# Performance work log

Hardware: AMD Instinct MI355X
Metric: run time of the kernel (lower is better)

## Reference

```python
import math
import jax, jax.numpy as jnp
import numpy as np

VOCAB = 50257
HIDDEN = 768
TYPE_VOCAB = 2
MAX_POS = 5000
EPS = 1e-12


def sinusoidal_pe(max_len, dim):
    # matches SinPositionalEncoding: pe[:,0::2]=sin(pos*div), pe[:,1::2]=cos(pos*div)
    position = np.arange(max_len, dtype=np.float32)[:, None]
    div_term = np.exp(np.arange(0, dim, 2, dtype=np.float32) * -(math.log(10000.0) / dim))
    pe = np.zeros((max_len, dim), dtype=np.float32)
    pe[:, 0::2] = np.sin(position * div_term)
    pe[:, 1::2] = np.cos(position * div_term)
    return jnp.asarray(pe)  # [max_len, dim]


def setup_inputs() -> dict:
    key = jax.random.key(0)
    k1, k2, k3, k4, k5 = jax.random.split(key, 5)
    B, N = 8, 4096
    return {
        "input_ids": jax.random.randint(k1, (B, N), 0, VOCAB, dtype=jnp.int64 if jax.config.jax_enable_x64 else jnp.int32),
        "tok_struct_vec": jax.random.randint(k2, (B, N, 3), 0, MAX_POS, dtype=jnp.int32),
        "token_type_ids": jax.random.randint(k3, (B, N), 0, TYPE_VOCAB, dtype=jnp.int32),
        "word_emb": jax.random.normal(k4, (VOCAB, HIDDEN), dtype=jnp.float32) * 0.02,
        "type_emb": jax.random.normal(k5, (TYPE_VOCAB, HIDDEN), dtype=jnp.float32) * 0.02,
        "gamma": jnp.ones((HIDDEN,), dtype=jnp.float32),
        "beta": jnp.zeros((HIDDEN,), dtype=jnp.float32),
    }


def reference(input_ids, tok_struct_vec, token_type_ids, word_emb, type_emb, gamma, beta):
    B, N = input_ids.shape
    pe = sinusoidal_pe(MAX_POS, HIDDEN)  # [max_pos, H]

    words = word_emb[input_ids]                      # [B,N,H] gather
    types = type_emb[token_type_ids]                 # [B,N,H] gather
    pos = jnp.broadcast_to(pe[:N][None], (B, N, HIDDEN))  # pe[:, :n].expand

    # compute_se: vectorized gather of pe rows by structure positions
    para = pe[tok_struct_vec[:, :, 0]]               # [B,N,H]
    sent = pe[tok_struct_vec[:, :, 1]]
    tok = pe[tok_struct_vec[:, :, 2]]
    struct = para + sent + tok                       # tok_se_comb_mode == 'sum'

    emb = words + pos + types + struct
    # BertLayerNorm (eps=1e-12); dropout is identity in eval
    mean = jnp.mean(emb, axis=-1, keepdims=True)
    var = jnp.mean(jnp.square(emb - mean), axis=-1, keepdims=True)
    out = (emb - mean) / jnp.sqrt(var + EPS) * gamma + beta
    return out
```

## Files before the change

### kernel.cpp

```cpp
#include <hip/hip_runtime.h>
#include <hip/hip_fp16.h>
#include <cstdint>
#include <cmath>

#define HIDDEN   768
#define NPAIR    (HIDDEN / 2)
#define SEQ_N    4096
#define LN_EPS   1e-12f
#define N_HI     80
#define N_LO     64

typedef float    f4v __attribute__((ext_vector_type(4)));
typedef _Float16 h4v __attribute__((ext_vector_type(4)));

__global__ __launch_bounds__(256) void pe_tables_kernel(__half2* __restrict__ T) {
    const int total = (N_HI + N_LO) * NPAIR;
    int idx = blockIdx.x * 256 + threadIdx.x;
    if (idx >= total) return;
    int r = idx / NPAIR;
    int i = idx % NPAIR;
    const float L = logf(10000.0f) / (float)HIDDEN;
    float div = expf(-2.0f * (float)i * L);
    int p = (r < N_HI) ? (r << 6) : (r - N_HI);
    float s, c;
    sincosf((float)p * div, &s, &c);
    T[idx] = __floats2half2_rn(s, c);
}

__device__ __forceinline__ void pe_acc(float4& x, const h4v a, const h4v b) {
    const float sA0 = (float)a.x, cA0 = (float)a.y, sA1 = (float)a.z, cA1 = (float)a.w;
    const float sB0 = (float)b.x, cB0 = (float)b.y, sB1 = (float)b.z, cB1 = (float)b.w;
    x.x = fmaf(sA0, cB0, fmaf(cA0, sB0, x.x));
    x.y = fmaf(cA0, cB0, fmaf(-sA0, sB0, x.y));
    x.z = fmaf(sA1, cB1, fmaf(cA1, sB1, x.z));
    x.w = fmaf(cA1, cB1, fmaf(-sA1, sB1, x.w));
}

__global__ __launch_bounds__(256) void emb_ln_kernel(
    const int*     __restrict__ ids,
    const int*     __restrict__ svec,
    const int*     __restrict__ tt,
    const float*   __restrict__ word_emb,
    const float*   __restrict__ type_emb,
    const float*   __restrict__ gamma,
    const float*   __restrict__ beta,
    const __half2* __restrict__ T,
    float*         __restrict__ out,
    int n_tokens)
{
    const int wave = threadIdx.x >> 6;
    const int lane = threadIdx.x & 63;
    const int tok  = blockIdx.x * 4 + wave;
    if (tok >= n_tokens) return;

    const int n  = tok & (SEQ_N - 1);
    const int id = ids[tok];
    const int ty = tt[tok];
    const int p0 = svec[tok * 3 + 0];
    const int p1 = svec[tok * 3 + 1];
    const int p2 = svec[tok * 3 + 2];

    const float4* wrow = reinterpret_cast<const float4*>(word_emb + (size_t)id * HIDDEN);
    const float4* trow = reinterpret_cast<const float4*>(type_emb + (size_t)ty * HIDDEN);

    #define T1ROW(p) reinterpret_cast<const h4v*>(T + (size_t)((p) >> 6) * NPAIR)
    #define T2ROW(p) reinterpret_cast<const h4v*>(T + (size_t)(N_HI + ((p) & 63)) * NPAIR)
    const h4v* A0 = T1ROW(n),  *B0 = T2ROW(n);
    const h4v* A1 = T1ROW(p0), *B1 = T2ROW(p0);
    const h4v* A2 = T1ROW(p1), *B2 = T2ROW(p1);
    const h4v* A3 = T1ROW(p2), *B3 = T2ROW(p2);
    #undef T1ROW
    #undef T2ROW

    float4 acc[3];
    float s = 0.0f, ss = 0.0f;

    #pragma unroll
    for (int k = 0; k < 3; ++k) {
        const int d4 = lane + 64 * k;

        float4 w = wrow[d4];
        float4 t = trow[d4];
        h4v a0 = A0[d4], b0 = B0[d4];
        h4v a1 = A1[d4], b1 = B1[d4];
        h4v a2 = A2[d4], b2 = B2[d4];
        h4v a3 = A3[d4], b3 = B3[d4];

        float4 x;
        x.x = w.x + t.x; x.y = w.y + t.y; x.z = w.z + t.z; x.w = w.w + t.w;
        pe_acc(x, a0, b0);
        pe_acc(x, a1, b1);
        pe_acc(x, a2, b2);
        pe_acc(x, a3, b3);

        acc[k] = x;
        s  += x.x + x.y + x.z + x.w;
        ss += x.x * x.x + x.y * x.y + x.z * x.z + x.w * x.w;
    }

    #pragma unroll
    for (int off = 1; off < 64; off <<= 1) {
        s  += __shfl_xor(s,  off);
        ss += __shfl_xor(ss, off);
    }

    const float mean = s * (1.0f / (float)HIDDEN);
    const float var  = ss * (1.0f / (float)HIDDEN) - mean * mean;
    const float inv  = rsqrtf(var + LN_EPS);

    const float4* g4 = reinterpret_cast<const float4*>(gamma);
    const float4* b4 = reinterpret_cast<const float4*>(beta);
    float4* orow = reinterpret_cast<float4*>(out + (size_t)tok * HIDDEN);

    #pragma unroll
    for (int k = 0; k < 3; ++k) {
        const int d4 = lane + 64 * k;
        const float4 g = g4[d4];
        const float4 b = b4[d4];
        const float4 x = acc[k];
        float4 r;
        r.x = (x.x - mean) * inv * g.x + b.x;
        r.y = (x.y - mean) * inv * g.y + b.y;
        r.z = (x.z - mean) * inv * g.z + b.z;
        r.w = (x.w - mean) * inv * g.w + b.w;
        orow[d4] = r;
    }
}

extern "C" void kernel_launch(void* const* d_in, const int* in_sizes, int n_in,
                              void* d_out, int out_size, void* d_ws, size_t ws_size,
                              hipStream_t stream) {
    const int*   ids      = (const int*)d_in[0];
    const int*   svec     = (const int*)d_in[1];
    const int*   tt       = (const int*)d_in[2];
    const float* word_emb = (const float*)d_in[3];
    const float* type_emb = (const float*)d_in[4];
    const float* gamma    = (const float*)d_in[5];
    const float* beta     = (const float*)d_in[6];
    float*       out      = (float*)d_out;

    const int n_tokens = in_sizes[0];
    const int grid_main = (n_tokens + 3) / 4;

    __half2* T = (__half2*)d_ws;
    const int total_tab = (N_HI + N_LO) * NPAIR;
    pe_tables_kernel<<<(total_tab + 255) / 256, 256, 0, stream>>>(T);
    emb_ln_kernel<<<grid_main, 256, 0, stream>>>(
        ids, svec, tt, word_emb, type_emb, gamma, beta, T, out, n_tokens);
}
```

Before: 53.25 us.

## Use persistent grid-stride waves with prefetch of next token's indices

```diff
diff --git a/kernel.cpp b/kernel.cpp
--- a/kernel.cpp
+++ b/kernel.cpp
@@ -9,6 +9,7 @@
 #define LN_EPS   1e-12f
 #define N_HI     80
 #define N_LO     64
+#define NBLK     2048
 
 typedef float    f4v __attribute__((ext_vector_type(4)));
 typedef _Float16 h4v __attribute__((ext_vector_type(4)));
@@ -36,7 +37,7 @@
     x.w = fmaf(cA1, cB1, fmaf(-sA1, sB1, x.w));
 }
 
-__global__ __launch_bounds__(256) void emb_ln_kernel(
+__global__ __launch_bounds__(256, 8) void emb_ln_kernel(
     const int*     __restrict__ ids,
     const int*     __restrict__ svec,
     const int*     __restrict__ tt,
@@ -50,80 +51,93 @@
 {
     const int wave = threadIdx.x >> 6;
     const int lane = threadIdx.x & 63;
-    const int tok  = blockIdx.x * 4 + wave;
+    const int nw   = NBLK * 4;
+    int tok = blockIdx.x * 4 + wave;
     if (tok >= n_tokens) return;
 
-    const int n  = tok & (SEQ_N - 1);
-    const int id = ids[tok];
-    const int ty = tt[tok];
-    const int p0 = svec[tok * 3 + 0];
-    const int p1 = svec[tok * 3 + 1];
-    const int p2 = svec[tok * 3 + 2];
+    int tu = __builtin_amdgcn_readfirstlane(tok);
+    int id = ids[tu], ty = tt[tu];
+    int p0 = svec[3 * tu], p1 = svec[3 * tu + 1], p2 = svec[3 * tu + 2];
 
-    const float4* wrow = reinterpret_cast<const float4*>(word_emb + (size_t)id * HIDDEN);
-    const float4* trow = reinterpret_cast<const float4*>(type_emb + (size_t)ty * HIDDEN);
+    for (;;) {
+        const int n = tu & (SEQ_N - 1);
 
-    #define T1ROW(p) reinterpret_cast<const h4v*>(T + (size_t)((p) >> 6) * NPAIR)
-    #define T2ROW(p) reinterpret_cast<const h4v*>(T + (size_t)(N_HI + ((p) & 63)) * NPAIR)
-    const h4v* A0 = T1ROW(n),  *B0 = T2ROW(n);
-    const h4v* A1 = T1ROW(p0), *B1 = T2ROW(p0);
-    const h4v* A2 = T1ROW(p1), *B2 = T2ROW(p1);
-    const h4v* A3 = T1ROW(p2), *B3 = T2ROW(p2);
-    #undef T1ROW
-    #undef T2ROW
+        const float4* wrow = reinterpret_cast<const float4*>(word_emb + (size_t)id * HIDDEN);
+        const float4* trow = reinterpret_cast<const float4*>(type_emb + (size_t)ty * HIDDEN);
 
-    float4 acc[3];
-    float s = 0.0f, ss = 0.0f;
+        #define T1ROW(p) reinterpret_cast<const h4v*>(T + (size_t)((p) >> 6) * NPAIR)
+        #define T2ROW(p) reinterpret_cast<const h4v*>(T + (size_t)(N_HI + ((p) & 63)) * NPAIR)
+        const h4v* A0 = T1ROW(n),  *B0 = T2ROW(n);
+        const h4v* A1 = T1ROW(p0), *B1 = T2ROW(p0);
+        const h4v* A2 = T1ROW(p1), *B2 = T2ROW(p1);
+        const h4v* A3 = T1ROW(p2), *B3 = T2ROW(p2);
+        #undef T1ROW
+        #undef T2ROW
 
-    #pragma unroll
-    for (int k = 0; k < 3; ++k) {
-        const int d4 = lane + 64 * k;
+        const int tnext = tu + nw;
+        const bool more = tnext < n_tokens;
+        int id_n = 0, ty_n = 0, q0 = 0, q1 = 0, q2 = 0;
+        if (more) {
+            id_n = ids[tnext]; ty_n = tt[tnext];
+            q0 = svec[3 * tnext]; q1 = svec[3 * tnext + 1]; q2 = svec[3 * tnext + 2];
+        }
 
-        float4 w = wrow[d4];
-        float4 t = trow[d4];
-        h4v a0 = A0[d4], b0 = B0[d4];
-        h4v a1 = A1[d4], b1 = B1[d4];
-        h4v a2 = A2[d4], b2 = B2[d4];
-        h4v a3 = A3[d4], b3 = B3[d4];
+        float4 acc[3];
+        float s = 0.0f, ss = 0.0f;
 
-        float4 x;
-        x.x = w.x + t.x; x.y = w.y + t.y; x.z = w.z + t.z; x.w = w.w + t.w;
-        pe_acc(x, a0, b0);
-        pe_acc(x, a1, b1);
-        pe_acc(x, a2, b2);
-        pe_acc(x, a3, b3);
+        #pragma unroll
+        for (int k = 0; k < 3; ++k) {
+            const int d4 = lane + 64 * k;
 
-        acc[k] = x;
-        s  += x.x + x.y + x.z + x.w;
-        ss += x.x * x.x + x.y * x.y + x.z * x.z + x.w * x.w;
-    }
+            float4 w = wrow[d4];
+            float4 t = trow[d4];
+            h4v a0 = A0[d4], b0 = B0[d4];
+            h4v a1 = A1[d4], b1 = B1[d4];
+            h4v a2 = A2[d4], b2 = B2[d4];
+            h4v a3 = A3[d4], b3 = B3[d4];
 
-    #pragma unroll
-    for (int off = 1; off < 64; off <<= 1) {
-        s  += __shfl_xor(s,  off);
-        ss += __shfl_xor(ss, off);
-    }
+            float4 x;
+            x.x = w.x + t.x; x.y = w.y + t.y; x.z = w.z + t.z; x.w = w.w + t.w;
+            pe_acc(x, a0, b0);
+            pe_acc(x, a1, b1);
+            pe_acc(x, a2, b2);
+            pe_acc(x, a3, b3);
 
-    const float mean = s * (1.0f / (float)HIDDEN);
-    const float var  = ss * (1.0f / (float)HIDDEN) - mean * mean;
-    const float inv  = rsqrtf(var + LN_EPS);
+            acc[k] = x;
+            s  += x.x + x.y + x.z + x.w;
+            ss += x.x * x.x + x.y * x.y + x.z * x.z + x.w * x.w;
+        }
 
-    const float4* g4 = reinterpret_cast<const float4*>(gamma);
-    const float4* b4 = reinterpret_cast<const float4*>(beta);
-    float4* orow = reinterpret_cast<float4*>(out + (size_t)tok * HIDDEN);
+        #pragma unroll
+        for (int off = 1; off < 64; off <<= 1) {
+            s  += __shfl_xor(s,  off);
+            ss += __shfl_xor(ss, off);
+        }
 
-    #pragma unroll
-    for (int k = 0; k < 3; ++k) {
-        const int d4 = lane + 64 * k;
-        const float4 g = g4[d4];
-        const float4 b = b4[d4];
-        const float4 x = acc[k];
-        float4 r;
-        r.x = (x.x - mean) * inv * g.x + b.x;
-        r.y = (x.y - mean) * inv * g.y + b.y;
-        r.z = (x.z - mean) * inv * g.z + b.z;
-        r.w = (x.w - mean) * inv * g.w + b.w;
-        orow[d4] = r;
+        const float mean = s * (1.0f / (float)HIDDEN);
+        const float var  = ss * (1.0f / (float)HIDDEN) - mean * mean;
+        const float inv  = rsqrtf(var + LN_EPS);
+
+        const float4* g4 = reinterpret_cast<const float4*>(gamma);
+        const float4* b4 = reinterpret_cast<const float4*>(beta);
+        float4* orow = reinterpret_cast<float4*>(out + (size_t)tu * HIDDEN);
+
+        #pragma unroll
+        for (int k = 0; k < 3; ++k) {
+            const int d4 = lane + 64 * k;
+            const float4 g = g4[d4];
+            const float4 b = b4[d4];
+            const float4 x = acc[k];
+            float4 r;
+            r.x = (x.x - mean) * inv * g.x + b.x;
+            r.y = (x.y - mean) * inv * g.y + b.y;
+            r.z = (x.z - mean) * inv * g.z + b.z;
+            r.w = (x.w - mean) * inv * g.w + b.w;
+            orow[d4] = r;
+        }
+
+        if (!more) break;
+        tu = tnext; id = id_n; ty = ty_n; p0 = q0; p1 = q1; p2 = q2;
     }
 }
 
@@ -140,11 +154,10 @@
     float*       out      = (float*)d_out;
 
     const int n_tokens = in_sizes[0];
-    const int grid_main = (n_tokens + 3) / 4;
 
     __half2* T = (__half2*)d_ws;
     const int total_tab = (N_HI + N_LO) * NPAIR;
     pe_tables_kernel<<<(total_tab + 255) / 256, 256, 0, stream>>>(T);
-    emb_ln_kernel<<<grid_main, 256, 0, stream>>>(
+    emb_ln_kernel<<<NBLK, 256, 0, stream>>>(
         ids, svec, tt, word_emb, type_emb, gamma, beta, T, out, n_tokens);
 }
```

Result: slower. 120.5 us (+126.2%).
